# Performance work log

Measured on AMD Instinct MI355X. Metric: run time of the kernel, lower is better.

Reference implementation:

```python
import jax, jax.numpy as jnp
import numpy as np

B = 4096
D = 512
N_CLASSES = 100
TEMPERATURE = 0.5


def setup_inputs() -> dict:
    key = jax.random.key(0)
    k1, k2, k3 = jax.random.split(key, 3)
    emb_i = jax.random.normal(k1, (B, D), dtype=jnp.float32)
    emb_j = jax.random.normal(k2, (B, D), dtype=jnp.float32)
    target = jax.random.randint(k3, (B,), 0, N_CLASSES, dtype=jnp.int64)
    return {"emb_i": emb_i, "emb_j": emb_j, "target": target}


def _l2_normalize(x, eps=1e-12):
    # matches torch F.normalize(dim=1): x / max(||x||, eps)
    n = jnp.sqrt(jnp.sum(x * x, axis=1, keepdims=True))
    return x / jnp.maximum(n, eps)


def reference(emb_i, emb_j, target):
    size = emb_i.shape[0]          # B
    n2 = 2 * size                  # 2B
    t = jnp.float32(TEMPERATURE)

    z_i = _l2_normalize(emb_i)
    z_j = _l2_normalize(emb_j)
    reps = jnp.concatenate([z_i, z_j], axis=0)                 # [2B, D]
    sim = jnp.matmul(reps, reps.T)                             # [2B, 2B]

    # positives: diag at offsets +B and -B
    sim_ij = jnp.diagonal(sim, offset=size)                    # [B]
    sim_ji = jnp.diagonal(sim, offset=-size)                   # [B]
    positives = jnp.concatenate([sim_ij, sim_ji], axis=0)      # [2B]
    nominator = jnp.exp(positives / t)

    idx = jnp.arange(n2)
    labels = jnp.concatenate([target, target])                 # [2B]
    # sample_mask: zero where same label AND |i-j| != B (also zeros the diagonal)
    same_label = labels[:, None] == labels[None, :]
    not_pos_pair = jnp.abs(idx[:, None] - idx[None, :]) != size
    sample_mask = jnp.where(same_label & not_pos_pair, 0.0, 1.0).astype(jnp.float32)
    # negatives_mask: ~eye
    neg_mask = 1.0 - jnp.eye(n2, dtype=jnp.float32)

    denom = jnp.sum(sample_mask * neg_mask * jnp.exp(sim / t), axis=1)  # [2B]
    loss_partial = -jnp.log(nominator / (denom + 1e-7))
    loss = jnp.sum(loss_partial) / n2
    return loss
```

## Files before the change

### kernel.cpp

```cpp
#include <hip/hip_runtime.h>
#include <hip/hip_bf16.h>
#include <cstdint>

#define B_SIZE 4096
#define TWO_B  8192
#define DIM    512
#define NPAIRS 2080
#define EXP_SCALE 2.8853900817779268f

typedef __attribute__((ext_vector_type(4))) float f32x4;

#define WAITVM(n) __builtin_amdgcn_s_waitcnt(0xF70 | (n))
#define BARRIER() __builtin_amdgcn_s_barrier()

__device__ __forceinline__ void async16(const void* g, void* l) {
    __builtin_amdgcn_global_load_lds(
        (const __attribute__((address_space(1))) unsigned int*)g,
        (__attribute__((address_space(3))) unsigned int*)l,
        16, 0, 0);
}

__global__ __launch_bounds__(256) void norm_pos_kernel(
    const float* __restrict__ emb_i, const float* __restrict__ emb_j,
    unsigned char* __restrict__ reps, float* __restrict__ pos,
    float* __restrict__ denom, float* __restrict__ out)
{
    int t = threadIdx.x, b0 = blockIdx.x;
    int lane = t & 63, w = t >> 6;
    int gz = b0 * 256 + t;
    if (gz < TWO_B) denom[gz] = 0.0f;
    if (b0 == 32 && t == 0) out[0] = 0.0f;

    #pragma unroll
    for (int it = 0; it < 4; it++) {
        int b = b0 * 4 + w + it * 1024;
        const float4* ri = (const float4*)(emb_i + (size_t)b * DIM);
        const float4* rj = (const float4*)(emb_j + (size_t)b * DIM);
        float4 xi0 = ri[lane * 2], xi1 = ri[lane * 2 + 1];
        float4 xj0 = rj[lane * 2], xj1 = rj[lane * 2 + 1];
        float si = xi0.x*xi0.x + xi0.y*xi0.y + xi0.z*xi0.z + xi0.w*xi0.w
                 + xi1.x*xi1.x + xi1.y*xi1.y + xi1.z*xi1.z + xi1.w*xi1.w;
        float sj = xj0.x*xj0.x + xj0.y*xj0.y + xj0.z*xj0.z + xj0.w*xj0.w
                 + xj1.x*xj1.x + xj1.y*xj1.y + xj1.z*xj1.z + xj1.w*xj1.w;
        #pragma unroll
        for (int o = 1; o < 64; o <<= 1) { si += __shfl_xor(si, o, 64); sj += __shfl_xor(sj, o, 64); }
        float rni = 1.0f / fmaxf(sqrtf(si), 1e-12f);
        float rnj = 1.0f / fmaxf(sqrtf(sj), 1e-12f);
        float4 zi0, zi1, zj0, zj1;
        zi0.x = xi0.x*rni; zi0.y = xi0.y*rni; zi0.z = xi0.z*rni; zi0.w = xi0.w*rni;
        zi1.x = xi1.x*rni; zi1.y = xi1.y*rni; zi1.z = xi1.z*rni; zi1.w = xi1.w*rni;
        zj0.x = xj0.x*rnj; zj0.y = xj0.y*rnj; zj0.z = xj0.z*rnj; zj0.w = xj0.w*rnj;
        zj1.x = xj1.x*rnj; zj1.y = xj1.y*rnj; zj1.z = xj1.z*rnj; zj1.w = xj1.w*rnj;
        int a0 = __builtin_amdgcn_cvt_pk_fp8_f32(zi0.x, zi0.y, 0, false);
        a0     = __builtin_amdgcn_cvt_pk_fp8_f32(zi0.z, zi0.w, a0, true);
        int a1 = __builtin_amdgcn_cvt_pk_fp8_f32(zi1.x, zi1.y, 0, false);
        a1     = __builtin_amdgcn_cvt_pk_fp8_f32(zi1.z, zi1.w, a1, true);
        int b0p = __builtin_amdgcn_cvt_pk_fp8_f32(zj0.x, zj0.y, 0, false);
        b0p    = __builtin_amdgcn_cvt_pk_fp8_f32(zj0.z, zj0.w, b0p, true);
        int b1 = __builtin_amdgcn_cvt_pk_fp8_f32(zj1.x, zj1.y, 0, false);
        b1     = __builtin_amdgcn_cvt_pk_fp8_f32(zj1.z, zj1.w, b1, true);
        ((int2*)(reps + (size_t)b * DIM))[lane]            = make_int2(a0, a1);
        ((int2*)(reps + (size_t)(b + B_SIZE) * DIM))[lane] = make_int2(b0p, b1);
        float d = zi0.x*zj0.x + zi0.y*zj0.y + zi0.z*zj0.z + zi0.w*zj0.w
                + zi1.x*zj1.x + zi1.y*zj1.y + zi1.z*zj1.z + zi1.w*zj1.w;
        #pragma unroll
        for (int o = 1; o < 64; o <<= 1) d += __shfl_xor(d, o, 64);
        if (lane == 0) pos[b] = d;
    }
}

#define BM 128
#define BK 64
#define KITERS 8

__global__ __launch_bounds__(256) void sim_denom_kernel(
    const unsigned char* __restrict__ reps,
    const int* __restrict__ target,
    float* __restrict__ denom)
{
    __shared__ __align__(16) unsigned char As0[BM * BK];
    __shared__ __align__(16) unsigned char As1[BM * BK];
    __shared__ __align__(16) unsigned char Bs0[BM * BK];
    __shared__ __align__(16) unsigned char Bs1[BM * BK];

    int t = threadIdx.x;
    int raw = blockIdx.x;
    int id = (raw & 7) * 260 + (raw >> 3);

    const int sI[10]  = {0,0,0,0,1,1,1,2,2,3};
    const int sJ[10]  = {0,1,2,3,1,2,3,2,3,3};
    const int off[11] = {0,136,392,648,904,1040,1296,1552,1688,1944,2080};
    int s = 0;
    while (off[s + 1] <= id) s++;
    int l = id - off[s];
    int u, v;
    if (sI[s] == sJ[s]) {
        u = 0;
        while (((u + 1) * (32 - u)) / 2 <= l) u++;
        v = u + (l - (u * (33 - u)) / 2);
    } else { u = l >> 4; v = l & 15; }
    int bi = sI[s] * 16 + u;
    int bj = sJ[s] * 16 + v;
    int brow = bi * BM;
    int bcol = bj * BM;

    int wave = t >> 6, lane = t & 63;
    int wr = wave >> 1, wc = wave & 1;
    int quad = lane >> 4, lm = lane & 15;

    f32x4 acc[4][4];
    #pragma unroll
    for (int i = 0; i < 4; i++)
        #pragma unroll
        for (int j = 0; j < 4; j++) acc[i][j] = (f32x4)0.0f;

    int srow = t >> 2;
    int sp   = (t & 3) ^ ((srow ^ (srow >> 2)) & 3);
    const unsigned char* gA = reps + (size_t)(brow + srow) * DIM + sp * 16;
    const unsigned char* gB = reps + (size_t)(bcol + srow) * DIM + sp * 16;

    auto stage = [&](unsigned char* Ab, unsigned char* Bb, int k0) {
        #pragma unroll
        for (int c = 0; c < 2; c++) {
            async16(gA + k0 + c * 64 * DIM, Ab + t * 16 + c * 4096);
            async16(gB + k0 + c * 64 * DIM, Bb + t * 16 + c * 4096);
        }
    };
    auto compute = [&](const unsigned char* Ab, const unsigned char* Bb) {
        #pragma unroll
        for (int ss = 0; ss < 2; ss++) {
            long af[4], bf[4];
            #pragma unroll
            for (int mi = 0; mi < 4; mi++) {
                int rl = wr * 64 + mi * 16 + lm;
                int p = (ss * 2 + (quad >> 1)) ^ ((rl ^ (rl >> 2)) & 3);
                af[mi] = *(const long*)(Ab + rl * 64 + p * 16 + (quad & 1) * 8);
            }
            #pragma unroll
            for (int ni = 0; ni < 4; ni++) {
                int cl = wc * 64 + ni * 16 + lm;
                int p = (ss * 2 + (quad >> 1)) ^ ((cl ^ (cl >> 2)) & 3);
                bf[ni] = *(const long*)(Bb + cl * 64 + p * 16 + (quad & 1) * 8);
            }
            #pragma unroll
            for (int mi = 0; mi < 4; mi++)
                #pragma unroll
                for (int ni = 0; ni < 4; ni++)
                    acc[mi][ni] = __builtin_amdgcn_mfma_f32_16x16x32_fp8_fp8(
                        af[mi], bf[ni], acc[mi][ni], 0, 0, 0);
        }
    };

    stage(As0, Bs0, 0);
    stage(As1, Bs1, BK);

    #pragma unroll
    for (int k = 0; k < KITERS; k++) {
        unsigned char* Ac = (k & 1) ? As1 : As0;
        unsigned char* Bc = (k & 1) ? Bs1 : Bs0;
        if (k < KITERS - 1) WAITVM(4); else WAITVM(0);
        BARRIER();
        compute(Ac, Bc);
        BARRIER();
        if (k + 2 < KITERS) stage(Ac, Bc, (k + 2) * BK);
    }

    bool haspos = (bj - bi == 32);
    int labc[4];
    #pragma unroll
    for (int ni = 0; ni < 4; ni++)
        labc[ni] = target[(bcol + wc * 64 + ni * 16 + lm) & (B_SIZE - 1)];

    float colacc[4] = {0.f, 0.f, 0.f, 0.f};
    #pragma unroll
    for (int mi = 0; mi < 4; mi++) {
        #pragma unroll
        for (int r = 0; r < 4; r++) {
            int rl = wr * 64 + mi * 16 + quad * 4 + r;
            int labr = target[(brow + rl) & (B_SIZE - 1)];
            float rowacc = 0.0f;
            #pragma unroll
            for (int ni = 0; ni < 4; ni++) {
                int cl = wc * 64 + ni * 16 + lm;
                bool pospair = haspos && (rl == cl);
                bool masked = (labr == labc[ni]) && !pospair;
                float e = masked ? 0.0f
                                 : __builtin_amdgcn_exp2f(acc[mi][ni][r] * EXP_SCALE);
                rowacc += e;
                colacc[ni] += e;
            }
            rowacc += __shfl_xor(rowacc, 1, 64);
            rowacc += __shfl_xor(rowacc, 2, 64);
            rowacc += __shfl_xor(rowacc, 4, 64);
            rowacc += __shfl_xor(rowacc, 8, 64);
            if (lm == 0) atomicAdd(&denom[brow + rl], rowacc);
        }
    }
    if (bi != bj) {
        #pragma unroll
        for (int ni = 0; ni < 4; ni++) {
            float c = colacc[ni];
            c += __shfl_xor(c, 16, 64);
            c += __shfl_xor(c, 32, 64);
            if (lane < 16) atomicAdd(&denom[bcol + wc * 64 + ni * 16 + lm], c);
        }
    }
}

__global__ __launch_bounds__(256) void loss_kernel(
    const float* __restrict__ denom, const float* __restrict__ pos,
    float* __restrict__ out)
{
    __shared__ float sc[4];
    int t = threadIdx.x, b = blockIdx.x;
    int i = b * 256 + t;
    float v = logf(denom[i] + 1e-7f);
    float p = (i < B_SIZE) ? pos[i] : 0.0f;
    float v2 = v - 4.0f * p;
    #pragma unroll
    for (int o = 32; o > 0; o >>= 1) v2 += __shfl_down(v2, o, 64);
    int lane = t & 63, w = t >> 6;
    if (lane == 0) sc[w] = v2;
    __syncthreads();
    if (t == 0) atomicAdd(out, (sc[0] + sc[1] + sc[2] + sc[3]) * (1.0f / (float)TWO_B));
}

extern "C" void kernel_launch(void* const* d_in, const int* in_sizes, int n_in,
                              void* d_out, int out_size, void* d_ws, size_t ws_size,
                              hipStream_t stream)
{
    const float* emb_i  = (const float*)d_in[0];
    const float* emb_j  = (const float*)d_in[1];
    const int*   target = (const int*)d_in[2];
    float* out = (float*)d_out;

    char* ws = (char*)d_ws;
    unsigned char* reps = (unsigned char*)ws;
    float* pos   = (float*)(ws + (size_t)TWO_B * DIM);
    float* denom = (float*)(ws + (size_t)TWO_B * DIM + B_SIZE * 4);

    norm_pos_kernel<<<256, 256, 0, stream>>>(emb_i, emb_j, reps, pos, denom, out);
    sim_denom_kernel<<<NPAIRS, 256, 0, stream>>>(reps, target, denom);
    loss_kernel<<<TWO_B / 256, 256, 0, stream>>>(denom, pos, out);
}
```

Measured before the change: 131.9 us.

## Load MFMA fragments directly from global memory, dropping LDS staging

Removes the LDS double buffering with async global-to-LDS loads and barriers. Each lane now loads its 8-byte fp8 A/B fragments straight from global memory into registers, ping-ponging between two register sets one k-step ahead. The interleaved block-id swizzle is also dropped in favour of the plain block index. This saves LDS traffic and barriers but loses data sharing across waves, so each wave fetches its fragments with narrow 8-byte strided loads that lean on L1/L2, and the prefetch distance is short.

Result: slower. 223.7 us (+69.6%).

```diff
diff --git a/kernel.cpp b/kernel.cpp
--- a/kernel.cpp
+++ b/kernel.cpp
@@ -9,16 +9,6 @@
 #define EXP_SCALE 2.8853900817779268f
 
 typedef __attribute__((ext_vector_type(4))) float f32x4;
-
-#define WAITVM(n) __builtin_amdgcn_s_waitcnt(0xF70 | (n))
-#define BARRIER() __builtin_amdgcn_s_barrier()
-
-__device__ __forceinline__ void async16(const void* g, void* l) {
-    __builtin_amdgcn_global_load_lds(
-        (const __attribute__((address_space(1))) unsigned int*)g,
-        (__attribute__((address_space(3))) unsigned int*)l,
-        16, 0, 0);
-}
 
 __global__ __launch_bounds__(256) void norm_pos_kernel(
     const float* __restrict__ emb_i, const float* __restrict__ emb_j,
@@ -55,12 +45,12 @@
         a0     = __builtin_amdgcn_cvt_pk_fp8_f32(zi0.z, zi0.w, a0, true);
         int a1 = __builtin_amdgcn_cvt_pk_fp8_f32(zi1.x, zi1.y, 0, false);
         a1     = __builtin_amdgcn_cvt_pk_fp8_f32(zi1.z, zi1.w, a1, true);
-        int b0p = __builtin_amdgcn_cvt_pk_fp8_f32(zj0.x, zj0.y, 0, false);
-        b0p    = __builtin_amdgcn_cvt_pk_fp8_f32(zj0.z, zj0.w, b0p, true);
-        int b1 = __builtin_amdgcn_cvt_pk_fp8_f32(zj1.x, zj1.y, 0, false);
-        b1     = __builtin_amdgcn_cvt_pk_fp8_f32(zj1.z, zj1.w, b1, true);
+        int c0 = __builtin_amdgcn_cvt_pk_fp8_f32(zj0.x, zj0.y, 0, false);
+        c0     = __builtin_amdgcn_cvt_pk_fp8_f32(zj0.z, zj0.w, c0, true);
+        int c1 = __builtin_amdgcn_cvt_pk_fp8_f32(zj1.x, zj1.y, 0, false);
+        c1     = __builtin_amdgcn_cvt_pk_fp8_f32(zj1.z, zj1.w, c1, true);
         ((int2*)(reps + (size_t)b * DIM))[lane]            = make_int2(a0, a1);
-        ((int2*)(reps + (size_t)(b + B_SIZE) * DIM))[lane] = make_int2(b0p, b1);
+        ((int2*)(reps + (size_t)(b + B_SIZE) * DIM))[lane] = make_int2(c0, c1);
         float d = zi0.x*zj0.x + zi0.y*zj0.y + zi0.z*zj0.z + zi0.w*zj0.w
                 + zi1.x*zj1.x + zi1.y*zj1.y + zi1.z*zj1.z + zi1.w*zj1.w;
         #pragma unroll
@@ -70,22 +60,15 @@
 }
 
 #define BM 128
-#define BK 64
-#define KITERS 8
+#define KSTEPS 16
 
 __global__ __launch_bounds__(256) void sim_denom_kernel(
     const unsigned char* __restrict__ reps,
     const int* __restrict__ target,
     float* __restrict__ denom)
 {
-    __shared__ __align__(16) unsigned char As0[BM * BK];
-    __shared__ __align__(16) unsigned char As1[BM * BK];
-    __shared__ __align__(16) unsigned char Bs0[BM * BK];
-    __shared__ __align__(16) unsigned char Bs1[BM * BK];
-
     int t = threadIdx.x;
-    int raw = blockIdx.x;
-    int id = (raw & 7) * 260 + (raw >> 3);
+    int id = blockIdx.x;
 
     const int sI[10]  = {0,0,0,0,1,1,1,2,2,3};
     const int sJ[10]  = {0,1,2,3,1,2,3,2,3,3};
@@ -114,55 +97,52 @@
         #pragma unroll
         for (int j = 0; j < 4; j++) acc[i][j] = (f32x4)0.0f;
 
-    int srow = t >> 2;
-    int sp   = (t & 3) ^ ((srow ^ (srow >> 2)) & 3);
-    const unsigned char* gA = reps + (size_t)(brow + srow) * DIM + sp * 16;
-    const unsigned char* gB = reps + (size_t)(bcol + srow) * DIM + sp * 16;
-
-    auto stage = [&](unsigned char* Ab, unsigned char* Bb, int k0) {
-        #pragma unroll
-        for (int c = 0; c < 2; c++) {
-            async16(gA + k0 + c * 64 * DIM, Ab + t * 16 + c * 4096);
-            async16(gB + k0 + c * 64 * DIM, Bb + t * 16 + c * 4096);
-        }
-    };
-    auto compute = [&](const unsigned char* Ab, const unsigned char* Bb) {
-        #pragma unroll
-        for (int ss = 0; ss < 2; ss++) {
-            long af[4], bf[4];
-            #pragma unroll
-            for (int mi = 0; mi < 4; mi++) {
-                int rl = wr * 64 + mi * 16 + lm;
-                int p = (ss * 2 + (quad >> 1)) ^ ((rl ^ (rl >> 2)) & 3);
-                af[mi] = *(const long*)(Ab + rl * 64 + p * 16 + (quad & 1) * 8);
-            }
-            #pragma unroll
-            for (int ni = 0; ni < 4; ni++) {
-                int cl = wc * 64 + ni * 16 + lm;
-                int p = (ss * 2 + (quad >> 1)) ^ ((cl ^ (cl >> 2)) & 3);
-                bf[ni] = *(const long*)(Bb + cl * 64 + p * 16 + (quad & 1) * 8);
+    const unsigned char* pA[4];
+    const unsigned char* pB[4];
+    #pragma unroll
+    for (int mi = 0; mi < 4; mi++)
+        pA[mi] = reps + (size_t)(brow + wr * 64 + mi * 16 + lm) * DIM + quad * 8;
+    #pragma unroll
+    for (int ni = 0; ni < 4; ni++)
+        pB[ni] = reps + (size_t)(bcol + wc * 64 + ni * 16 + lm) * DIM + quad * 8;
+
+    long afA[4], bfA[4], afB[4], bfB[4];
+    #pragma unroll
+    for (int x = 0; x < 4; x++) {
+        afA[x] = *(const long*)(pA[x]);
+        bfA[x] = *(const long*)(pB[x]);
+    }
+    #pragma unroll
+    for (int k = 0; k < KSTEPS; k++) {
+        if ((k & 1) == 0) {
+            if (k + 1 < KSTEPS) {
+                #pragma unroll
+                for (int x = 0; x < 4; x++) {
+                    afB[x] = *(const long*)(pA[x] + (k + 1) * 32);
+                    bfB[x] = *(const long*)(pB[x] + (k + 1) * 32);
+                }
             }
             #pragma unroll
             for (int mi = 0; mi < 4; mi++)
                 #pragma unroll
                 for (int ni = 0; ni < 4; ni++)
                     acc[mi][ni] = __builtin_amdgcn_mfma_f32_16x16x32_fp8_fp8(
-                        af[mi], bf[ni], acc[mi][ni], 0, 0, 0);
+                        afA[mi], bfA[ni], acc[mi][ni], 0, 0, 0);
+        } else {
+            if (k + 1 < KSTEPS) {
+                #pragma unroll
+                for (int x = 0; x < 4; x++) {
+                    afA[x] = *(const long*)(pA[x] + (k + 1) * 32);
+                    bfA[x] = *(const long*)(pB[x] + (k + 1) * 32);
+                }
+            }
+            #pragma unroll
+            for (int mi = 0; mi < 4; mi++)
+                #pragma unroll
+                for (int ni = 0; ni < 4; ni++)
+                    acc[mi][ni] = __builtin_amdgcn_mfma_f32_16x16x32_fp8_fp8(
+                        afB[mi], bfB[ni], acc[mi][ni], 0, 0, 0);
         }
-    };
-
-    stage(As0, Bs0, 0);
-    stage(As1, Bs1, BK);
-
-    #pragma unroll
-    for (int k = 0; k < KITERS; k++) {
-        unsigned char* Ac = (k & 1) ? As1 : As0;
-        unsigned char* Bc = (k & 1) ? Bs1 : Bs0;
-        if (k < KITERS - 1) WAITVM(4); else WAITVM(0);
-        BARRIER();
-        compute(Ac, Bc);
-        BARRIER();
-        if (k + 2 < KITERS) stage(Ac, Bc, (k + 2) * BK);
     }
 
     bool haspos = (bj - bi == 32);
```

## Fuse loss reduction into sim kernel via last-block counter and widen norm grid

Applied to the files above, without the earlier changes.

Removes the separate loss kernel by having the last-finishing block of the similarity kernel (detected via an atomic counter) compute the log-sum and write the loss. The normalization kernel now processes one row per wave with 4x more blocks instead of looping. The XCD-aware block index swizzle is dropped. This saves a launch and increases parallelism in the norm stage, but adds a serial tail reduction in one block and may lose cache locality from the swizzle.

New measurement: 306.4 us. 2.32x slower.

```diff
diff --git a/kernel.cpp b/kernel.cpp
--- a/kernel.cpp
+++ b/kernel.cpp
@@ -23,50 +23,47 @@
 __global__ __launch_bounds__(256) void norm_pos_kernel(
     const float* __restrict__ emb_i, const float* __restrict__ emb_j,
     unsigned char* __restrict__ reps, float* __restrict__ pos,
-    float* __restrict__ denom, float* __restrict__ out)
+    float* __restrict__ denom, int* __restrict__ cnt, float* __restrict__ out)
 {
     int t = threadIdx.x, b0 = blockIdx.x;
     int lane = t & 63, w = t >> 6;
     int gz = b0 * 256 + t;
     if (gz < TWO_B) denom[gz] = 0.0f;
-    if (b0 == 32 && t == 0) out[0] = 0.0f;
-
-    #pragma unroll
-    for (int it = 0; it < 4; it++) {
-        int b = b0 * 4 + w + it * 1024;
-        const float4* ri = (const float4*)(emb_i + (size_t)b * DIM);
-        const float4* rj = (const float4*)(emb_j + (size_t)b * DIM);
-        float4 xi0 = ri[lane * 2], xi1 = ri[lane * 2 + 1];
-        float4 xj0 = rj[lane * 2], xj1 = rj[lane * 2 + 1];
-        float si = xi0.x*xi0.x + xi0.y*xi0.y + xi0.z*xi0.z + xi0.w*xi0.w
-                 + xi1.x*xi1.x + xi1.y*xi1.y + xi1.z*xi1.z + xi1.w*xi1.w;
-        float sj = xj0.x*xj0.x + xj0.y*xj0.y + xj0.z*xj0.z + xj0.w*xj0.w
-                 + xj1.x*xj1.x + xj1.y*xj1.y + xj1.z*xj1.z + xj1.w*xj1.w;
-        #pragma unroll
-        for (int o = 1; o < 64; o <<= 1) { si += __shfl_xor(si, o, 64); sj += __shfl_xor(sj, o, 64); }
-        float rni = 1.0f / fmaxf(sqrtf(si), 1e-12f);
-        float rnj = 1.0f / fmaxf(sqrtf(sj), 1e-12f);
-        float4 zi0, zi1, zj0, zj1;
-        zi0.x = xi0.x*rni; zi0.y = xi0.y*rni; zi0.z = xi0.z*rni; zi0.w = xi0.w*rni;
-        zi1.x = xi1.x*rni; zi1.y = xi1.y*rni; zi1.z = xi1.z*rni; zi1.w = xi1.w*rni;
-        zj0.x = xj0.x*rnj; zj0.y = xj0.y*rnj; zj0.z = xj0.z*rnj; zj0.w = xj0.w*rnj;
-        zj1.x = xj1.x*rnj; zj1.y = xj1.y*rnj; zj1.z = xj1.z*rnj; zj1.w = xj1.w*rnj;
-        int a0 = __builtin_amdgcn_cvt_pk_fp8_f32(zi0.x, zi0.y, 0, false);
-        a0     = __builtin_amdgcn_cvt_pk_fp8_f32(zi0.z, zi0.w, a0, true);
-        int a1 = __builtin_amdgcn_cvt_pk_fp8_f32(zi1.x, zi1.y, 0, false);
-        a1     = __builtin_amdgcn_cvt_pk_fp8_f32(zi1.z, zi1.w, a1, true);
-        int b0p = __builtin_amdgcn_cvt_pk_fp8_f32(zj0.x, zj0.y, 0, false);
-        b0p    = __builtin_amdgcn_cvt_pk_fp8_f32(zj0.z, zj0.w, b0p, true);
-        int b1 = __builtin_amdgcn_cvt_pk_fp8_f32(zj1.x, zj1.y, 0, false);
-        b1     = __builtin_amdgcn_cvt_pk_fp8_f32(zj1.z, zj1.w, b1, true);
-        ((int2*)(reps + (size_t)b * DIM))[lane]            = make_int2(a0, a1);
-        ((int2*)(reps + (size_t)(b + B_SIZE) * DIM))[lane] = make_int2(b0p, b1);
-        float d = zi0.x*zj0.x + zi0.y*zj0.y + zi0.z*zj0.z + zi0.w*zj0.w
-                + zi1.x*zj1.x + zi1.y*zj1.y + zi1.z*zj1.z + zi1.w*zj1.w;
-        #pragma unroll
-        for (int o = 1; o < 64; o <<= 1) d += __shfl_xor(d, o, 64);
-        if (lane == 0) pos[b] = d;
-    }
+    if (b0 == 32 && t == 0) { cnt[0] = 0; out[0] = 0.0f; }
+
+    int b = b0 * 4 + w;
+    const float4* ri = (const float4*)(emb_i + (size_t)b * DIM);
+    const float4* rj = (const float4*)(emb_j + (size_t)b * DIM);
+    float4 xi0 = ri[lane * 2], xi1 = ri[lane * 2 + 1];
+    float4 xj0 = rj[lane * 2], xj1 = rj[lane * 2 + 1];
+    float si = xi0.x*xi0.x + xi0.y*xi0.y + xi0.z*xi0.z + xi0.w*xi0.w
+             + xi1.x*xi1.x + xi1.y*xi1.y + xi1.z*xi1.z + xi1.w*xi1.w;
+    float sj = xj0.x*xj0.x + xj0.y*xj0.y + xj0.z*xj0.z + xj0.w*xj0.w
+             + xj1.x*xj1.x + xj1.y*xj1.y + xj1.z*xj1.z + xj1.w*xj1.w;
+    #pragma unroll
+    for (int o = 1; o < 64; o <<= 1) { si += __shfl_xor(si, o, 64); sj += __shfl_xor(sj, o, 64); }
+    float rni = 1.0f / fmaxf(sqrtf(si), 1e-12f);
+    float rnj = 1.0f / fmaxf(sqrtf(sj), 1e-12f);
+    float4 zi0, zi1, zj0, zj1;
+    zi0.x = xi0.x*rni; zi0.y = xi0.y*rni; zi0.z = xi0.z*rni; zi0.w = xi0.w*rni;
+    zi1.x = xi1.x*rni; zi1.y = xi1.y*rni; zi1.z = xi1.z*rni; zi1.w = xi1.w*rni;
+    zj0.x = xj0.x*rnj; zj0.y = xj0.y*rnj; zj0.z = xj0.z*rnj; zj0.w = xj0.w*rnj;
+    zj1.x = xj1.x*rnj; zj1.y = xj1.y*rnj; zj1.z = xj1.z*rnj; zj1.w = xj1.w*rnj;
+    int a0 = __builtin_amdgcn_cvt_pk_fp8_f32(zi0.x, zi0.y, 0, false);
+    a0     = __builtin_amdgcn_cvt_pk_fp8_f32(zi0.z, zi0.w, a0, true);
+    int a1 = __builtin_amdgcn_cvt_pk_fp8_f32(zi1.x, zi1.y, 0, false);
+    a1     = __builtin_amdgcn_cvt_pk_fp8_f32(zi1.z, zi1.w, a1, true);
+    int c0 = __builtin_amdgcn_cvt_pk_fp8_f32(zj0.x, zj0.y, 0, false);
+    c0     = __builtin_amdgcn_cvt_pk_fp8_f32(zj0.z, zj0.w, c0, true);
+    int c1 = __builtin_amdgcn_cvt_pk_fp8_f32(zj1.x, zj1.y, 0, false);
+    c1     = __builtin_amdgcn_cvt_pk_fp8_f32(zj1.z, zj1.w, c1, true);
+    ((int2*)(reps + (size_t)b * DIM))[lane]            = make_int2(a0, a1);
+    ((int2*)(reps + (size_t)(b + B_SIZE) * DIM))[lane] = make_int2(c0, c1);
+    float d = zi0.x*zj0.x + zi0.y*zj0.y + zi0.z*zj0.z + zi0.w*zj0.w
+            + zi1.x*zj1.x + zi1.y*zj1.y + zi1.z*zj1.z + zi1.w*zj1.w;
+    #pragma unroll
+    for (int o = 1; o < 64; o <<= 1) d += __shfl_xor(d, o, 64);
+    if (lane == 0) pos[b] = d;
 }
 
 #define BM 128
@@ -76,7 +73,10 @@
 __global__ __launch_bounds__(256) void sim_denom_kernel(
     const unsigned char* __restrict__ reps,
     const int* __restrict__ target,
-    float* __restrict__ denom)
+    float* __restrict__ denom,
+    const float* __restrict__ pos,
+    int* __restrict__ cnt,
+    float* __restrict__ out)
 {
     __shared__ __align__(16) unsigned char As0[BM * BK];
     __shared__ __align__(16) unsigned char As1[BM * BK];
@@ -84,8 +84,7 @@
     __shared__ __align__(16) unsigned char Bs1[BM * BK];
 
     int t = threadIdx.x;
-    int raw = blockIdx.x;
-    int id = (raw & 7) * 260 + (raw >> 3);
+    int id = blockIdx.x;
 
     const int sI[10]  = {0,0,0,0,1,1,1,2,2,3};
     const int sJ[10]  = {0,1,2,3,1,2,3,2,3,3};
@@ -205,24 +204,32 @@
             if (lane < 16) atomicAdd(&denom[bcol + wc * 64 + ni * 16 + lm], c);
         }
     }
-}
-
-__global__ __launch_bounds__(256) void loss_kernel(
-    const float* __restrict__ denom, const float* __restrict__ pos,
-    float* __restrict__ out)
-{
-    __shared__ float sc[4];
-    int t = threadIdx.x, b = blockIdx.x;
-    int i = b * 256 + t;
-    float v = logf(denom[i] + 1e-7f);
-    float p = (i < B_SIZE) ? pos[i] : 0.0f;
-    float v2 = v - 4.0f * p;
-    #pragma unroll
-    for (int o = 32; o > 0; o >>= 1) v2 += __shfl_down(v2, o, 64);
-    int lane = t & 63, w = t >> 6;
-    if (lane == 0) sc[w] = v2;
+
     __syncthreads();
-    if (t == 0) atomicAdd(out, (sc[0] + sc[1] + sc[2] + sc[3]) * (1.0f / (float)TWO_B));
+    __threadfence();
+    int* is_last = (int*)Bs0;
+    if (t == 0) {
+        int c = __hip_atomic_fetch_add(cnt, 1, __ATOMIC_ACQ_REL, __HIP_MEMORY_SCOPE_AGENT);
+        *is_last = (c == NPAIRS - 1);
+    }
+    __syncthreads();
+    if (*is_last) {
+        __threadfence();
+        float* sc = (float*)As0;
+        float vsum = 0.0f;
+        for (int i = t; i < TWO_B; i += 256) {
+            float dn = __hip_atomic_load(&denom[i], __ATOMIC_RELAXED, __HIP_MEMORY_SCOPE_AGENT);
+            vsum += logf(dn + 1e-7f);
+        }
+        float psum = 0.0f;
+        for (int i = t; i < B_SIZE; i += 256) psum += pos[i];
+        float v2 = vsum - 4.0f * psum;
+        #pragma unroll
+        for (int o = 1; o < 64; o <<= 1) v2 += __shfl_xor(v2, o, 64);
+        if (lane == 0) sc[wave] = v2;
+        __syncthreads();
+        if (t == 0) out[0] = (sc[0] + sc[1] + sc[2] + sc[3]) * (1.0f / (float)TWO_B);
+    }
 }
 
 extern "C" void kernel_launch(void* const* d_in, const int* in_sizes, int n_in,
@@ -238,8 +245,8 @@
     unsigned char* reps = (unsigned char*)ws;
     float* pos   = (float*)(ws + (size_t)TWO_B * DIM);
     float* denom = (float*)(ws + (size_t)TWO_B * DIM + B_SIZE * 4);
-
-    norm_pos_kernel<<<256, 256, 0, stream>>>(emb_i, emb_j, reps, pos, denom, out);
-    sim_denom_kernel<<<NPAIRS, 256, 0, stream>>>(reps, target, denom);
-    loss_kernel<<<TWO_B / 256, 256, 0, stream>>>(denom, pos, out);
-}
+    int*   cnt   = (int*)  (ws + (size_t)TWO_B * DIM + B_SIZE * 4 + TWO_B * 4);
+
+    norm_pos_kernel<<<1024, 256, 0, stream>>>(emb_i, emb_j, reps, pos, denom, cnt, out);
+    sim_denom_kernel<<<NPAIRS, 256, 0, stream>>>(reps, target, denom, pos, cnt, out);
+}
```
